# Performance work log

Hardware: AMD Instinct MI355X
Metric: run time of the kernel (lower is better)

## Reference

```python
import jax, jax.numpy as jnp
import numpy as np

OUT_LEN = 60


def lstm_cell(h, c, x_t, Wih, Whh, b):
    # PyTorch gate ordering: i, f, g, o
    gates = x_t @ Wih.T + h @ Whh.T + b  # [B, 4H]
    i, f, g, o = jnp.split(gates, 4, axis=-1)
    c_new = jax.nn.sigmoid(f) * c + jax.nn.sigmoid(i) * jnp.tanh(g)
    h_new = jax.nn.sigmoid(o) * jnp.tanh(c_new)
    return h_new, c_new


def _forward(x, enc_Wih, enc_Whh, enc_bih, enc_bhh,
             dec_Wih, dec_Whh, dec_bih, dec_bhh, proj_W, proj_b):
    B = x.shape[0]
    H = enc_Whh.shape[1]
    enc_b = enc_bih + enc_bhh
    dec_b = dec_bih + dec_bhh

    # ---- encoder LSTM over time ----
    h0 = jnp.zeros((B, H), x.dtype)
    c0 = jnp.zeros((B, H), x.dtype)

    def enc_step(carry, x_t):
        h, c = carry
        h, c = lstm_cell(h, c, x_t, enc_Wih, enc_Whh, enc_b)
        return (h, c), None

    (h, c), _ = jax.lax.scan(enc_step, (h0, c0), jnp.swapaxes(x, 0, 1))

    inp0 = x[:, -1, :2]  # last observed (x, y)

    def dec_step(carry, _):
        h, c, inp = carry
        h, c = lstm_cell(h, c, inp, dec_Wih, dec_Whh, dec_b)
        pred = h @ proj_W.T + proj_b  # [B, 2]
        return (h, c, jax.lax.stop_gradient(pred)), pred

    _, preds = jax.lax.scan(dec_step, (h, c, inp0), None, length=OUT_LEN)
    return jnp.swapaxes(preds, 0, 1)  # [B, OUT_LEN, 2]


def setup_inputs() -> dict:
    key = jax.random.key(0)
    ks = jax.random.split(key, 12)
    B, T, D_IN, H, D_OUT = 8192, 50, 6, 128, 2
    s = 1.0 / np.sqrt(H)

    def u(k, shape):
        return jax.random.uniform(k, shape, jnp.float32, -s, s)

    return {
        "x": jax.random.normal(ks[0], (B, T, D_IN), jnp.float32),
        "enc_Wih": u(ks[1], (4 * H, D_IN)),
        "enc_Whh": u(ks[2], (4 * H, H)),
        "enc_bih": u(ks[3], (4 * H,)),
        "enc_bhh": u(ks[4], (4 * H,)),
        "dec_Wih": u(ks[5], (4 * H, D_OUT)),
        "dec_Whh": u(ks[6], (4 * H, H)),
        "dec_bih": u(ks[7], (4 * H,)),
        "dec_bhh": u(ks[8], (4 * H,)),
        "proj_W": u(ks[9], (D_OUT, H)),
        "proj_b": u(ks[10], (D_OUT,)),
    }


def reference(x, enc_Wih, enc_Whh, enc_bih, enc_bhh,
              dec_Wih, dec_Whh, dec_bih, dec_bhh, proj_W, proj_b):
    return _forward(x, enc_Wih, enc_Whh, enc_bih, enc_bhh,
                    dec_Wih, dec_Whh, dec_bih, dec_bhh, proj_W, proj_b)
```

## Files before the change

### kernel.cpp

```cpp
#include <hip/hip_runtime.h>
#include <cstddef>

typedef __attribute__((ext_vector_type(8))) _Float16 half8;
typedef __attribute__((ext_vector_type(4))) _Float16 half4;
typedef __attribute__((ext_vector_type(4))) float floatx4;

namespace {
constexpr int kH = 128;
constexpr int kTEnc = 50;
constexpr int kTDec = 60;
constexpr int kRows = 32;
constexpr int kThreads = 512;
constexpr int kBTot = 8192;
constexpr int kWfBytes = 3 * 32 * 5 * 64 * 8 * 2;
}

__device__ __forceinline__ float fexp2(float x) {
    float r; asm("v_exp_f32 %0, %1" : "=v"(r) : "v"(x)); return r;
}
__device__ __forceinline__ float frcp(float x) {
    float r; asm("v_rcp_f32 %0, %1" : "=v"(r) : "v"(x)); return r;
}
__device__ __forceinline__ float clampf(float x, float lo, float hi) {
    return fminf(fmaxf(x, lo), hi);
}

__global__ void lstm_prep(const float* __restrict__ encWhh, const float* __restrict__ encWih,
                          const float* __restrict__ decWhh, const float* __restrict__ decWih,
                          const float* __restrict__ encbih, const float* __restrict__ encbhh,
                          const float* __restrict__ decbih, const float* __restrict__ decbhh,
                          const float* __restrict__ projW,  const float* __restrict__ projb,
                          _Float16* __restrict__ wf, float* __restrict__ bias_s) {
    int idx = blockIdx.x * 256 + threadIdx.x;
    const float L2E = 1.4426950408889634f;
    if (idx < 3 * 512) {
        int mat = idx / 512, g = idx & 511;
        int gtype = g >> 7;
        float sc = (gtype == 1) ? -L2E : (gtype == 2) ? 2.0f * L2E : L2E;
        float b = (mat == 0) ? (encbih[g] + encbhh[g]) : (decbih[g] + decbhh[g]);
        if (mat == 2) b += decWih[g * 2 + 0] * projb[0] + decWih[g * 2 + 1] * projb[1];
        bias_s[idx] = sc * b;
    }
    if (idx >= 3 * 32 * 5 * 64) return;
    const int lane = idx & 63;
    const int kc   = (idx >> 6) % 5;
    const int gt   = (idx / 320) & 31;
    const int mat  = idx / 10240;
    const float* Whh = (mat == 0) ? encWhh : decWhh;
    const float* Wih = (mat == 0) ? encWih : decWih;
    const int din = (mat == 0) ? 6 : (mat == 1) ? 2 : 0;
    const int g = gt * 16 + (lane & 15);
    const int gtype = g >> 7;
    const float sc = (gtype == 1) ? -L2E : (gtype == 2) ? 2.0f * L2E : L2E;

    _Float16 vals[8];
    #pragma unroll
    for (int j = 0; j < 8; j++) {
        int k = kc * 32 + (lane >> 4) * 8 + j;
        float v = 0.0f;
        if (k < kH) {
            v = Whh[g * kH + k];
            if (mat == 2)
                v += decWih[g * 2 + 0] * projW[k] + decWih[g * 2 + 1] * projW[kH + k];
            v *= sc;
        } else {
            int kk = k - kH;
            if (kk < din)                       v = sc * Wih[g * din + kk];
            else if (kk >= 8 && kk < 8 + din)   v = sc * Wih[g * din + (kk - 8)];
        }
        vals[j] = (_Float16)v;
    }
    *(half8*)(wf + (size_t)idx * 8) = *(half8*)vals;
}

__global__ __launch_bounds__(kThreads, 2) void lstm_main(
    const float* __restrict__ x,
    const _Float16* __restrict__ wf,
    const float* __restrict__ bias_s,
    const float* __restrict__ projW,
    const float* __restrict__ projb,
    float* __restrict__ out)
{
    __shared__ alignas(16) _Float16 xs[kTEnc][kRows][2][8];
    __shared__ alignas(16) _Float16 hbuf[2][kRows][kH];
    __shared__ alignas(16) _Float16 decf[kRows][2][8];
    __shared__ alignas(16) _Float16 zeros16[8];
    __shared__ alignas(8)  float partial[2][8][kRows][2];
    __shared__ float pb_s[2];

    const int tid  = threadIdx.x;
    const int lane = tid & 63;
    const int wv   = tid >> 6;
    const int l15  = lane & 15;
    const int l4   = lane >> 4;
    const int rowBase = blockIdx.x * kRows;

    for (int i = tid; i < kTEnc * kRows * 8; i += kThreads) {
        int d = i & 7;
        int r = (i >> 3) & (kRows - 1);
        int t = i >> 8;
        float v = (d < 6) ? x[(size_t)(rowBase + r) * (kTEnc * 6) + t * 6 + d] : 0.0f;
        _Float16 hi = (_Float16)v;
        xs[t][r][0][d] = hi;
        xs[t][r][1][d] = (_Float16)(v - (float)hi);
    }
    for (int i = tid; i < kRows * kH; i += kThreads)
        (&hbuf[0][0][0])[i] = (_Float16)0.0f;
    for (int i = tid; i < kRows * 16; i += kThreads)
        (&decf[0][0][0])[i] = (_Float16)0.0f;
    if (tid < 8)  zeros16[tid] = (_Float16)0.0f;
    if (tid < 2)  pb_s[tid] = projb[tid];

    floatx4 pwr[2];
    #pragma unroll
    for (int j = 0; j < 2; j++)
        pwr[j] = *(const floatx4*)(projW + j * kH + wv * 16 + l4 * 4);

    half8  wfr[4][5];
    floatx4 bs4[4];
    auto load_wb = [&](int mat) {
        #pragma unroll
        for (int gt = 0; gt < 4; gt++) {
            #pragma unroll
            for (int kc = 0; kc < 5; kc++) {
                size_t off = ((((size_t)mat * 32 + (gt * 8 + wv)) * 5 + kc) * 64 + lane) * 8;
                wfr[gt][kc] = *(const half8*)(wf + off);
            }
            bs4[gt] = *(const floatx4*)(bias_s + mat * 512 + gt * kH + wv * 16 + l4 * 4);
        }
    };
    load_wb(0);
    __syncthreads();

    float cst[2][4];
    float hreg[2][4];
    #pragma unroll
    for (int bt = 0; bt < 2; bt++)
        #pragma unroll
        for (int jj = 0; jj < 4; jj++) cst[bt][jj] = 0.0f;

    const int swz = (l15 & 7) << 4;
    int hoffs[4], woff;
    #pragma unroll
    for (int kc = 0; kc < 4; kc++)
        hoffs[kc] = (l15 * 256 + kc * 64 + l4 * 16) ^ swz;
    woff = (l15 * 256 + wv * 32 + l4 * 8) ^ swz;

    const char* encXbase = (l4 < 2) ? ((const char*)xs + l15 * 32 + l4 * 16) : (const char*)zeros16;
    const int   encXstep = (l4 < 2) ? (kRows * 2 * 8 * 2) : 0;
    const int   xbt      = (l4 < 2) ? 512 : 0;
    const char* decXaddr = (l4 < 2) ? ((const char*)decf + l15 * 32 + l4 * 16) : (const char*)zeros16;

    constexpr float kK2 = 2.8853900817779268f;

    auto run_step = [&](bool useX, half8 bx0, half8 bx1, int curBuf) {
        floatx4 acc[4][2];
        #pragma unroll
        for (int gt = 0; gt < 4; gt++) { acc[gt][0] = bs4[gt]; acc[gt][1] = bs4[gt]; }

        const char* baseH = (const char*)&hbuf[curBuf][0][0];
        #pragma unroll
        for (int kc = 0; kc < 4; kc++) {
            half8 b0 = *(const half8*)(baseH + hoffs[kc]);
            half8 b1 = *(const half8*)(baseH + hoffs[kc] + 4096);
            #pragma unroll
            for (int gt = 0; gt < 4; gt++) {
                acc[gt][0] = __builtin_amdgcn_mfma_f32_16x16x32_f16(wfr[gt][kc], b0, acc[gt][0], 0, 0, 0);
                acc[gt][1] = __builtin_amdgcn_mfma_f32_16x16x32_f16(wfr[gt][kc], b1, acc[gt][1], 0, 0, 0);
            }
        }
        if (useX) {
            #pragma unroll
            for (int gt = 0; gt < 4; gt++) {
                acc[gt][0] = __builtin_amdgcn_mfma_f32_16x16x32_f16(wfr[gt][4], bx0, acc[gt][0], 0, 0, 0);
                acc[gt][1] = __builtin_amdgcn_mfma_f32_16x16x32_f16(wfr[gt][4], bx1, acc[gt][1], 0, 0, 0);
            }
        }

        char* nH = (char*)&hbuf[curBuf ^ 1][0][0];
        #pragma unroll
        for (int bt = 0; bt < 2; bt++) {
            half4 pH;
            #pragma unroll
            for (int jj = 0; jj < 4; jj++) {
                float ai   = clampf(acc[0][bt][jj], -40.0f, 40.0f);
                float af   = clampf(acc[1][bt][jj], -40.0f, 40.0f);
                float ag   = clampf(acc[2][bt][jj], -40.0f, 40.0f);
                float ao   = clampf(acc[3][bt][jj], -40.0f, 40.0f);
                float e_i  = fexp2(ai);
                float e_mf = fexp2(af);
                float e_g  = fexp2(ag);
                float A    = (1.0f + e_i) * (1.0f + e_g);
                float r1   = frcp(A * (1.0f + e_mf));
                float cn   = r1 * fmaf(e_i * (e_g - 1.0f), 1.0f + e_mf, A * cst[bt][jj]);
                cst[bt][jj] = cn;
                float e_o  = fexp2(ao);
                float e_c  = fexp2(kK2 * clampf(cn, -30.0f, 30.0f));
                float r2   = frcp((1.0f + e_o) * (1.0f + e_c));
                float hn   = e_o * (e_c - 1.0f) * r2;
                hreg[bt][jj] = hn;
                pH[jj] = (_Float16)hn;
            }
            *(half4*)(nH + woff + bt * 4096) = pH;
        }
    };

    int cur = 0;

    for (int t = 0; t < kTEnc; t++) {
        const char* xb = encXbase + t * encXstep;
        half8 bx0 = *(const half8*)xb;
        half8 bx1 = *(const half8*)(xb + xbt);
        run_step(true, bx0, bx1, cur);
        __syncthreads();
        cur ^= 1;
    }

    auto proj_partial = [&](int par) {
        #pragma unroll
        for (int bt = 0; bt < 2; bt++) {
            float pp0 = hreg[bt][0] * pwr[0][0] + hreg[bt][1] * pwr[0][1]
                      + hreg[bt][2] * pwr[0][2] + hreg[bt][3] * pwr[0][3];
            float pp1 = hreg[bt][0] * pwr[1][0] + hreg[bt][1] * pwr[1][1]
                      + hreg[bt][2] * pwr[1][2] + hreg[bt][3] * pwr[1][3];
            pp0 += __shfl_xor(pp0, 16); pp0 += __shfl_xor(pp0, 32);
            pp1 += __shfl_xor(pp1, 16); pp1 += __shfl_xor(pp1, 32);
            if (l4 == 0) {
                partial[par][wv][bt * 16 + l15][0] = pp0;
                partial[par][wv][bt * 16 + l15][1] = pp1;
            }
        }
    };
    auto reduce_out = [&](int par, int t) {
        int r = lane >> 1, j = lane & 1;
        float s = pb_s[j];
        #pragma unroll
        for (int w8 = 0; w8 < 8; w8++) s += partial[par][w8][r][j];
        out[(size_t)(rowBase + r) * (kTDec * 2) + t * 2 + j] = s;
    };

    load_wb(1);
    if (tid < 2 * kRows) {
        int r = tid >> 1, j = tid & 1;
        decf[r][0][j] = xs[kTEnc - 1][r][0][j];
        decf[r][1][j] = xs[kTEnc - 1][r][1][j];
    }
    __syncthreads();
    {
        half8 bx0 = *(const half8*)decXaddr;
        half8 bx1 = *(const half8*)(decXaddr + xbt);
        run_step(true, bx0, bx1, cur);
        proj_partial(0);
        __syncthreads();
        cur ^= 1;
    }
    load_wb(2);

    half8 dummy = *(const half8*)zeros16;
    for (int t = 1; t < kTDec; t++) {
        if (wv == 0) reduce_out((t - 1) & 1, t - 1);
        run_step(false, dummy, dummy, cur);
        proj_partial(t & 1);
        __syncthreads();
        cur ^= 1;
    }
    if (wv == 0) reduce_out((kTDec - 1) & 1, kTDec - 1);
}

extern "C" void kernel_launch(void* const* d_in, const int* in_sizes, int n_in,
                              void* d_out, int out_size, void* d_ws, size_t ws_size,
                              hipStream_t stream) {
    const float* x      = (const float*)d_in[0];
    const float* encWih = (const float*)d_in[1];
    const float* encWhh = (const float*)d_in[2];
    const float* encbih = (const float*)d_in[3];
    const float* encbhh = (const float*)d_in[4];
    const float* decWih = (const float*)d_in[5];
    const float* decWhh = (const float*)d_in[6];
    const float* decbih = (const float*)d_in[7];
    const float* decbhh = (const float*)d_in[8];
    const float* projW  = (const float*)d_in[9];
    const float* projb  = (const float*)d_in[10];

    _Float16* wfrag = (_Float16*)d_ws;
    float* bias_s = (float*)((char*)d_ws + kWfBytes);
    float* out = (float*)d_out;

    lstm_prep<<<120, 256, 0, stream>>>(encWhh, encWih, decWhh, decWih,
                                       encbih, encbhh, decbih, decbhh,
                                       projW, projb, wfrag, bias_s);
    lstm_main<<<kBTot / kRows, kThreads, 0, stream>>>(x, wfrag, bias_s, projW, projb, out);
}
```

Before: 200.9 us.

## Software-pipeline two 16-row batch halves to overlap MFMA with gate activations

Splits the 32-row tile into two independent 16-row groups with separate double-buffered hidden states. Each phase issues one group's MFMAs while computing the other group's transcendental activations, so matrix and vector work can overlap across the recurrence. The decoder seed input is now loaded directly from global memory instead of copied from the staged encoder inputs. The cost is twice as many barriers per timestep and more complex scheduling and register pressure.

```diff
diff --git a/kernel.cpp b/kernel.cpp
--- a/kernel.cpp
+++ b/kernel.cpp
@@ -82,10 +82,10 @@
     float* __restrict__ out)
 {
     __shared__ alignas(16) _Float16 xs[kTEnc][kRows][2][8];
-    __shared__ alignas(16) _Float16 hbuf[2][kRows][kH];
+    __shared__ alignas(16) _Float16 hbuf[2][2][16][kH];
     __shared__ alignas(16) _Float16 decf[kRows][2][8];
     __shared__ alignas(16) _Float16 zeros16[8];
-    __shared__ alignas(8)  float partial[2][8][kRows][2];
+    __shared__ alignas(8)  float partial[2][8][16][2];
     __shared__ float pb_s[2];
 
     const int tid  = threadIdx.x;
@@ -104,12 +104,16 @@
         xs[t][r][0][d] = hi;
         xs[t][r][1][d] = (_Float16)(v - (float)hi);
     }
-    for (int i = tid; i < kRows * kH; i += kThreads)
-        (&hbuf[0][0][0])[i] = (_Float16)0.0f;
-    for (int i = tid; i < kRows * 16; i += kThreads)
-        (&decf[0][0][0])[i] = (_Float16)0.0f;
-    if (tid < 8)  zeros16[tid] = (_Float16)0.0f;
-    if (tid < 2)  pb_s[tid] = projb[tid];
+    for (int i = tid; i < 2 * 2 * 16 * kH; i += kThreads)
+        (&hbuf[0][0][0][0])[i] = (_Float16)0.0f;
+    {
+        int r = tid >> 4, hl = (tid >> 3) & 1, d = tid & 7;
+        float v = (d < 2) ? x[(size_t)(rowBase + r) * (kTEnc * 6) + (kTEnc - 1) * 6 + d] : 0.0f;
+        _Float16 hi = (_Float16)v;
+        decf[r][hl][d] = hl ? (_Float16)(v - (float)hi) : hi;
+    }
+    if (tid < 8) zeros16[tid] = (_Float16)0.0f;
+    if (tid < 2) pb_s[tid] = projb[tid];
 
     floatx4 pwr[2];
     #pragma unroll
@@ -132,139 +136,126 @@
     load_wb(0);
     __syncthreads();
 
-    float cst[2][4];
+    float cst[2][4] = {};
     float hreg[2][4];
-    #pragma unroll
-    for (int bt = 0; bt < 2; bt++)
-        #pragma unroll
-        for (int jj = 0; jj < 4; jj++) cst[bt][jj] = 0.0f;
+    floatx4 acc[2][4];
+    half8 bfr[4];
+    half8 bx;
+    int rd[2] = {0, 0};
 
     const int swz = (l15 & 7) << 4;
-    int hoffs[4], woff;
+    int hoffs[4];
     #pragma unroll
     for (int kc = 0; kc < 4; kc++)
         hoffs[kc] = (l15 * 256 + kc * 64 + l4 * 16) ^ swz;
-    woff = (l15 * 256 + wv * 32 + l4 * 8) ^ swz;
+    const int woff = (l15 * 256 + wv * 32 + l4 * 8) ^ swz;
 
     const char* encXbase = (l4 < 2) ? ((const char*)xs + l15 * 32 + l4 * 16) : (const char*)zeros16;
     const int   encXstep = (l4 < 2) ? (kRows * 2 * 8 * 2) : 0;
-    const int   xbt      = (l4 < 2) ? 512 : 0;
-    const char* decXaddr = (l4 < 2) ? ((const char*)decf + l15 * 32 + l4 * 16) : (const char*)zeros16;
+    const int   xgoff    = (l4 < 2) ? 512 : 0;
+    const char* decXbase = (l4 < 2) ? ((const char*)decf + l15 * 32 + l4 * 16) : (const char*)zeros16;
 
     constexpr float kK2 = 2.8853900817779268f;
 
-    auto run_step = [&](bool useX, half8 bx0, half8 bx1, int curBuf) {
-        floatx4 acc[4][2];
-        #pragma unroll
-        for (int gt = 0; gt < 4; gt++) { acc[gt][0] = bs4[gt]; acc[gt][1] = bs4[gt]; }
-
-        const char* baseH = (const char*)&hbuf[curBuf][0][0];
-        #pragma unroll
-        for (int kc = 0; kc < 4; kc++) {
-            half8 b0 = *(const half8*)(baseH + hoffs[kc]);
-            half8 b1 = *(const half8*)(baseH + hoffs[kc] + 4096);
+    auto LOADS = [&](int g) {
+        const char* b = (const char*)hbuf + g * 8192 + rd[g];
+        #pragma unroll
+        for (int kc = 0; kc < 4; kc++)
+            bfr[kc] = *(const half8*)(b + hoffs[kc]);
+    };
+    auto MFMA = [&](int g, bool hasX) {
+        #pragma unroll
+        for (int gt = 0; gt < 4; gt++) {
+            floatx4 a = __builtin_amdgcn_mfma_f32_16x16x32_f16(wfr[gt][0], bfr[0], bs4[gt], 0, 0, 0);
+            a = __builtin_amdgcn_mfma_f32_16x16x32_f16(wfr[gt][1], bfr[1], a, 0, 0, 0);
+            a = __builtin_amdgcn_mfma_f32_16x16x32_f16(wfr[gt][2], bfr[2], a, 0, 0, 0);
+            a = __builtin_amdgcn_mfma_f32_16x16x32_f16(wfr[gt][3], bfr[3], a, 0, 0, 0);
+            if (hasX)
+                a = __builtin_amdgcn_mfma_f32_16x16x32_f16(wfr[gt][4], bx, a, 0, 0, 0);
+            acc[g][gt] = a;
+        }
+    };
+    auto ACT = [&](int g) {
+        half4 pH;
+        #pragma unroll
+        for (int jj = 0; jj < 4; jj++) {
+            float ai   = clampf(acc[g][0][jj], -40.0f, 40.0f);
+            float af   = clampf(acc[g][1][jj], -40.0f, 40.0f);
+            float ag   = clampf(acc[g][2][jj], -40.0f, 40.0f);
+            float ao   = clampf(acc[g][3][jj], -40.0f, 40.0f);
+            float e_i  = fexp2(ai);
+            float e_mf = fexp2(af);
+            float e_g  = fexp2(ag);
+            float A    = (1.0f + e_i) * (1.0f + e_g);
+            float r1   = frcp(A * (1.0f + e_mf));
+            float cn   = r1 * fmaf(e_i * (e_g - 1.0f), 1.0f + e_mf, A * cst[g][jj]);
+            cst[g][jj] = cn;
+            float e_o  = fexp2(ao);
+            float e_c  = fexp2(kK2 * clampf(cn, -30.0f, 30.0f));
+            float r2   = frcp((1.0f + e_o) * (1.0f + e_c));
+            float hn   = e_o * (e_c - 1.0f) * r2;
+            hreg[g][jj] = hn;
+            pH[jj] = (_Float16)hn;
+        }
+        *(half4*)((char*)hbuf + g * 8192 + (rd[g] ^ 4096) + woff) = pH;
+        rd[g] ^= 4096;
+    };
+    auto PROJ = [&](int g) {
+        float pp0 = hreg[g][0] * pwr[0][0] + hreg[g][1] * pwr[0][1]
+                  + hreg[g][2] * pwr[0][2] + hreg[g][3] * pwr[0][3];
+        float pp1 = hreg[g][0] * pwr[1][0] + hreg[g][1] * pwr[1][1]
+                  + hreg[g][2] * pwr[1][2] + hreg[g][3] * pwr[1][3];
+        pp0 += __shfl_xor(pp0, 16); pp0 += __shfl_xor(pp0, 32);
+        pp1 += __shfl_xor(pp1, 16); pp1 += __shfl_xor(pp1, 32);
+        if (l4 == 0) {
+            partial[g][wv][l15][0] = pp0;
+            partial[g][wv][l15][1] = pp1;
+        }
+    };
+    auto REDUCE = [&](int g, int t) {
+        if (wv == 0 && lane < 32) {
+            int r = lane >> 1, j = lane & 1;
+            float s = pb_s[j];
             #pragma unroll
-            for (int gt = 0; gt < 4; gt++) {
-                acc[gt][0] = __builtin_amdgcn_mfma_f32_16x16x32_f16(wfr[gt][kc], b0, acc[gt][0], 0, 0, 0);
-                acc[gt][1] = __builtin_amdgcn_mfma_f32_16x16x32_f16(wfr[gt][kc], b1, acc[gt][1], 0, 0, 0);
-            }
-        }
-        if (useX) {
-            #pragma unroll
-            for (int gt = 0; gt < 4; gt++) {
-                acc[gt][0] = __builtin_amdgcn_mfma_f32_16x16x32_f16(wfr[gt][4], bx0, acc[gt][0], 0, 0, 0);
-                acc[gt][1] = __builtin_amdgcn_mfma_f32_16x16x32_f16(wfr[gt][4], bx1, acc[gt][1], 0, 0, 0);
-            }
-        }
-
-        char* nH = (char*)&hbuf[curBuf ^ 1][0][0];
-        #pragma unroll
-        for (int bt = 0; bt < 2; bt++) {
-            half4 pH;
-            #pragma unroll
-            for (int jj = 0; jj < 4; jj++) {
-                float ai   = clampf(acc[0][bt][jj], -40.0f, 40.0f);
-                float af   = clampf(acc[1][bt][jj], -40.0f, 40.0f);
-                float ag   = clampf(acc[2][bt][jj], -40.0f, 40.0f);
-                float ao   = clampf(acc[3][bt][jj], -40.0f, 40.0f);
-                float e_i  = fexp2(ai);
-                float e_mf = fexp2(af);
-                float e_g  = fexp2(ag);
-                float A    = (1.0f + e_i) * (1.0f + e_g);
-                float r1   = frcp(A * (1.0f + e_mf));
-                float cn   = r1 * fmaf(e_i * (e_g - 1.0f), 1.0f + e_mf, A * cst[bt][jj]);
-                cst[bt][jj] = cn;
-                float e_o  = fexp2(ao);
-                float e_c  = fexp2(kK2 * clampf(cn, -30.0f, 30.0f));
-                float r2   = frcp((1.0f + e_o) * (1.0f + e_c));
-                float hn   = e_o * (e_c - 1.0f) * r2;
-                hreg[bt][jj] = hn;
-                pH[jj] = (_Float16)hn;
-            }
-            *(half4*)(nH + woff + bt * 4096) = pH;
-        }
-    };
-
-    int cur = 0;
-
-    for (int t = 0; t < kTEnc; t++) {
-        const char* xb = encXbase + t * encXstep;
-        half8 bx0 = *(const half8*)xb;
-        half8 bx1 = *(const half8*)(xb + xbt);
-        run_step(true, bx0, bx1, cur);
-        __syncthreads();
-        cur ^= 1;
-    }
-
-    auto proj_partial = [&](int par) {
-        #pragma unroll
-        for (int bt = 0; bt < 2; bt++) {
-            float pp0 = hreg[bt][0] * pwr[0][0] + hreg[bt][1] * pwr[0][1]
-                      + hreg[bt][2] * pwr[0][2] + hreg[bt][3] * pwr[0][3];
-            float pp1 = hreg[bt][0] * pwr[1][0] + hreg[bt][1] * pwr[1][1]
-                      + hreg[bt][2] * pwr[1][2] + hreg[bt][3] * pwr[1][3];
-            pp0 += __shfl_xor(pp0, 16); pp0 += __shfl_xor(pp0, 32);
-            pp1 += __shfl_xor(pp1, 16); pp1 += __shfl_xor(pp1, 32);
-            if (l4 == 0) {
-                partial[par][wv][bt * 16 + l15][0] = pp0;
-                partial[par][wv][bt * 16 + l15][1] = pp1;
-            }
-        }
-    };
-    auto reduce_out = [&](int par, int t) {
-        int r = lane >> 1, j = lane & 1;
-        float s = pb_s[j];
-        #pragma unroll
-        for (int w8 = 0; w8 < 8; w8++) s += partial[par][w8][r][j];
-        out[(size_t)(rowBase + r) * (kTDec * 2) + t * 2 + j] = s;
-    };
-
+            for (int w8 = 0; w8 < 8; w8++) s += partial[g][w8][r][j];
+            out[(size_t)(rowBase + g * 16 + r) * (kTDec * 2) + t * 2 + j] = s;
+        }
+    };
+
+    LOADS(0); bx = *(const half8*)encXbase;
+    MFMA(0, true);
+    __syncthreads();
+    for (int t = 0; t < kTEnc - 1; t++) {
+        LOADS(1); bx = *(const half8*)(encXbase + t * encXstep + xgoff);
+        ACT(0); MFMA(1, true);
+        __syncthreads();
+        LOADS(0); bx = *(const half8*)(encXbase + (t + 1) * encXstep);
+        ACT(1); MFMA(0, true);
+        __syncthreads();
+    }
+    LOADS(1); bx = *(const half8*)(encXbase + (kTEnc - 1) * encXstep + xgoff);
+    ACT(0); MFMA(1, true);
     load_wb(1);
-    if (tid < 2 * kRows) {
-        int r = tid >> 1, j = tid & 1;
-        decf[r][0][j] = xs[kTEnc - 1][r][0][j];
-        decf[r][1][j] = xs[kTEnc - 1][r][1][j];
-    }
-    __syncthreads();
-    {
-        half8 bx0 = *(const half8*)decXaddr;
-        half8 bx1 = *(const half8*)(decXaddr + xbt);
-        run_step(true, bx0, bx1, cur);
-        proj_partial(0);
-        __syncthreads();
-        cur ^= 1;
-    }
+    __syncthreads();
+
+    LOADS(0); bx = *(const half8*)decXbase;
+    ACT(1); MFMA(0, true);
+    __syncthreads();
+    LOADS(1); bx = *(const half8*)(decXbase + xgoff);
+    ACT(0); PROJ(0); MFMA(1, true);
     load_wb(2);
-
-    half8 dummy = *(const half8*)zeros16;
-    for (int t = 1; t < kTDec; t++) {
-        if (wv == 0) reduce_out((t - 1) & 1, t - 1);
-        run_step(false, dummy, dummy, cur);
-        proj_partial(t & 1);
-        __syncthreads();
-        cur ^= 1;
-    }
-    if (wv == 0) reduce_out((kTDec - 1) & 1, kTDec - 1);
+    __syncthreads();
+
+    for (int d = 1; d < kTDec; d++) {
+        LOADS(0); ACT(1); PROJ(1); MFMA(0, false); REDUCE(0, d - 1);
+        __syncthreads();
+        LOADS(1); ACT(0); PROJ(0); MFMA(1, false); REDUCE(1, d - 1);
+        __syncthreads();
+    }
+    ACT(1); PROJ(1);
+    __syncthreads();
+    REDUCE(0, kTDec - 1);
+    REDUCE(1, kTDec - 1);
 }
 
 extern "C" void kernel_launch(void* const* d_in, const int* in_sizes, int n_in,
```

Measured after the change: 214.4 us. 1.07x slower.
